# Kernel optimization log

Measured on AMD Instinct MI355X. Metric: run time of the kernel, lower is better.

Reference implementation:

```python
import jax, jax.numpy as jnp
import numpy as np
from jax import lax

B, D, K = 256, 128, 8192


def _conv_same(x, w, b):
    # x: [B,C,H,W], w: [O,I,3,3] (torch Conv2d layout), stride 1, padding 1 == SAME
    y = lax.conv_general_dilated(x, w, (1, 1), 'SAME',
                                 dimension_numbers=('NCHW', 'OIHW', 'NCHW'))
    return y + b[None, :, None, None]


def _convT_same(x, w, b):
    # torch ConvTranspose2d(k=3, stride=1, padding=1) with weight [I,O,3,3]
    # == SAME conv with spatially flipped kernel and swapped in/out channels
    wt = jnp.flip(w, axis=(2, 3)).transpose(1, 0, 2, 3)  # -> [O,I,3,3]
    return _conv_same(x, wt, b)


def setup_inputs() -> dict:
    key = jax.random.key(0)
    ks = jax.random.split(key, 12)
    s = 0.05
    return {
        'patch':  jax.random.normal(ks[0], (B, 3, 64, 64), jnp.float32),
        'enc_w1': jax.random.normal(ks[1], (64, 3, 3, 3), jnp.float32) * s,
        'enc_b1': jnp.zeros((64,), jnp.float32),
        'enc_w2': jax.random.normal(ks[2], (D, 64, 3, 3), jnp.float32) * s,
        'enc_b2': jnp.zeros((D,), jnp.float32),
        'emb':    jax.random.normal(ks[3], (K, D), jnp.float32),
        'dec_w1': jax.random.normal(ks[4], (D, 64, 3, 3), jnp.float32) * s,  # ConvT [in,out,k,k]
        'dec_b1': jnp.zeros((64,), jnp.float32),
        'dec_w2': jax.random.normal(ks[5], (64, 64, 3, 3), jnp.float32) * s,
        'dec_b2': jnp.zeros((64,), jnp.float32),
        'dec_w3': jax.random.normal(ks[6], (64, 3, 3, 3), jnp.float32) * s,
        'dec_b3': jnp.zeros((3,), jnp.float32),
    }


def reference(patch, enc_w1, enc_b1, enc_w2, enc_b2, emb,
              dec_w1, dec_b1, dec_w2, dec_b2, dec_w3, dec_b3):
    # ---- encode_patch ----
    h = jax.nn.relu(_conv_same(patch, enc_w1, enc_b1))
    h = _conv_same(h, enc_w2, enc_b2)
    z = jnp.mean(h, axis=(2, 3))  # AdaptiveAvgPool2d((1,1)) + flatten -> [B,D]

    # ---- VQ: cdist + argmin + gather ----
    # argmin over squared L2 == argmin over cdist(p=2); avoid sqrt.
    d2 = (jnp.sum(z * z, axis=1, keepdims=True)
          + jnp.sum(emb * emb, axis=1)[None, :]
          - 2.0 * z @ emb.T)  # [B,K]
    encoding_indices = jnp.argmin(d2, axis=1)  # [B]
    z_q = emb[encoding_indices]  # [B,D]

    commitment_loss = jnp.mean((lax.stop_gradient(z_q) - z) ** 2)
    codebook_loss = jnp.mean((z_q - lax.stop_gradient(z)) ** 2)

    # ---- decode_vector ----
    # bilinear interpolate of a 1x1 map to 64x64 is a pure broadcast
    v = jnp.broadcast_to(z_q[:, :, None, None], (z_q.shape[0], z_q.shape[1], 64, 64))
    d = jax.nn.relu(_convT_same(v, dec_w1, dec_b1))
    d = jax.nn.relu(_convT_same(d, dec_w2, dec_b2))
    recon = jnp.tanh(_convT_same(d, dec_w3, dec_b3))  # [B,3,64,64]

    return recon, codebook_loss, commitment_loss, encoding_indices[:, None]
```

## Files before the change

### kernel.cpp

```cpp
#include <hip/hip_runtime.h>
#include <math.h>

typedef float float4u __attribute__((ext_vector_type(4), aligned(4)));


__global__ __launch_bounds__(256) void k_conv1_pre(
    const float* __restrict__ patch, const float* __restrict__ w1,
    const float* __restrict__ b1, const float* __restrict__ dw1,
    const float* __restrict__ emb, float* __restrict__ pstat,
    float* __restrict__ Wcfg, float* __restrict__ en2)
{
    __shared__ __align__(16) float lds[2304];
    const int blk = blockIdx.x;
    const int tid = threadIdx.x;

    if (blk >= 2048) {
        const int gid = (blk - 2048) * 256 + tid;
        if (gid < 73728) {
            const int cfg = gid >> 13;
            const int o = (gid >> 7) & 63;
            const int i = gid & 127;
            const int cy = cfg / 3, cx = cfg % 3;
            const int ylo = (cy == 2) ? 1 : 0, yhi = (cy == 0) ? 1 : 2;
            const int xlo = (cx == 2) ? 1 : 0, xhi = (cx == 0) ? 1 : 2;
            const float* wp = dw1 + ((size_t)i * 64 + o) * 9;
            float s = 0.f;
            for (int ky = ylo; ky <= yhi; ++ky)
                for (int kx = xlo; kx <= xhi; ++kx)
                    s += wp[ky * 3 + kx];
            Wcfg[gid] = s;
        } else if (gid < 81920) {
            const int k = gid - 73728;
            const float4* e = (const float4*)(emb + (size_t)k * 128);
            float s = 0.f;
            for (int t = 0; t < 32; ++t) {
                float4 v = e[t];
                s = fmaf(v.x, v.x, fmaf(v.y, v.y, fmaf(v.z, v.z, fmaf(v.w, v.w, s))));
            }
            en2[k] = s;
        }
        return;
    }

    const int b = blk >> 3, rg = blk & 7;
    const int y0 = rg * 8;
    const float* pb = patch + (size_t)b * 12288;
    for (int i = tid; i < 2160; i += 256) {
        const int c = i / 720, rem = i - c * 720;
        const int r = rem / 72, p = rem - r * 72;
        const int y = y0 + r - 1, x = p - 3;
        float v = 0.f;
        if (y >= 0 && y < 64 && x >= 0 && x < 64)
            v = pb[(c << 12) + (y << 6) + x];
        lds[i] = v;
    }
    __syncthreads();

    const int ch = tid & 63, q = tid >> 6;
    float w[3][3][3];
#pragma unroll
    for (int ic = 0; ic < 3; ++ic)
#pragma unroll
        for (int ky = 0; ky < 3; ++ky)
#pragma unroll
            for (int kx = 0; kx < 3; ++kx)
                w[ic][ky][kx] = w1[((ch * 3 + ic) * 3 + ky) * 3 + kx];
    const float bias = b1[ch];

    float T = 0, r0s = 0, r63s = 0, c0s = 0, c63s = 0;
    float h00 = 0, h063 = 0, h630 = 0, h6363 = 0;

#pragma unroll
    for (int sub = 0; sub < 2; ++sub) {
        const int yl = q * 2 + sub;
        const bool isr0  = (rg == 0) && (yl == 0);
        const bool isr63 = (rg == 7) && (yl == 7);
        float cr[3][3][2];
#pragma unroll
        for (int ic = 0; ic < 3; ++ic)
#pragma unroll
            for (int ky = 0; ky < 3; ++ky) {
                const float2 t2 = *(const float2*)&lds[(ic * 10 + yl + ky) * 72 + 2];
                cr[ic][ky][0] = t2.x; cr[ic][ky][1] = t2.y;
            }
#pragma unroll 4
        for (int xc = 0; xc < 16; ++xc) {
            float a0 = bias, a1 = bias, a2 = bias, a3 = bias;
#pragma unroll
            for (int ic = 0; ic < 3; ++ic)
#pragma unroll
                for (int ky = 0; ky < 3; ++ky) {
                    const float4 nw = *(const float4*)&lds[(ic * 10 + yl + ky) * 72 + xc * 4 + 4];
                    const float w0 = w[ic][ky][0], w1v = w[ic][ky][1], w2v = w[ic][ky][2];
                    a0 = fmaf(w0, cr[ic][ky][0], fmaf(w1v, cr[ic][ky][1], fmaf(w2v, nw.x, a0)));
                    a1 = fmaf(w0, cr[ic][ky][1], fmaf(w1v, nw.x, fmaf(w2v, nw.y, a1)));
                    a2 = fmaf(w0, nw.x, fmaf(w1v, nw.y, fmaf(w2v, nw.z, a2)));
                    a3 = fmaf(w0, nw.y, fmaf(w1v, nw.z, fmaf(w2v, nw.w, a3)));
                    cr[ic][ky][0] = nw.z; cr[ic][ky][1] = nw.w;
                }
            a0 = fmaxf(a0, 0.f); a1 = fmaxf(a1, 0.f);
            a2 = fmaxf(a2, 0.f); a3 = fmaxf(a3, 0.f);
            const float rs = (a0 + a1) + (a2 + a3);
            T += rs;
            if (isr0)  { r0s += rs;  if (xc == 0) h00 = a0;  if (xc == 15) h063 = a3; }
            if (isr63) { r63s += rs; if (xc == 0) h630 = a0; if (xc == 15) h6363 = a3; }
            if (xc == 0)  c0s += a0;
            if (xc == 15) c63s += a3;
        }
    }
    __syncthreads();
    {
        const float st[9] = {T, r0s, r63s, c0s, c63s, h00, h063, h630, h6363};
#pragma unroll
        for (int s = 0; s < 9; ++s) lds[(s * 4 + q) * 64 + ch] = st[s];
    }
    __syncthreads();
    if (tid < 64) {
        float* pp = pstat + (size_t)blk * 576;
#pragma unroll
        for (int s = 0; s < 9; ++s)
            pp[s * 64 + tid] = (lds[(s * 4 + 0) * 64 + tid] + lds[(s * 4 + 1) * 64 + tid])
                             + (lds[(s * 4 + 2) * 64 + tid] + lds[(s * 4 + 3) * 64 + tid]);
    }
}

__global__ __launch_bounds__(256) void k_zred(
    const float* __restrict__ pstat, const float* __restrict__ w2,
    const float* __restrict__ b2, float* __restrict__ z, float* __restrict__ zn2)
{
    __shared__ float fst[576];
    __shared__ __align__(16) float Ssh[576];
    __shared__ float zp[256];
    __shared__ float red2[128];
    const int b = blockIdx.x, tid = threadIdx.x;

    const float* pp = pstat + (size_t)b * 8 * 576;
    for (int i = tid; i < 576; i += 256) {
        float s = 0.f;
#pragma unroll
        for (int g = 0; g < 8; ++g) s += pp[g * 576 + i];
        fst[i] = s;
    }
    __syncthreads();

    if (tid < 64) {
        const float Tt   = fst[0 * 64 + tid], R0  = fst[1 * 64 + tid], R63 = fst[2 * 64 + tid];
        const float C0   = fst[3 * 64 + tid], C63 = fst[4 * 64 + tid];
        const float H00  = fst[5 * 64 + tid], H063 = fst[6 * 64 + tid];
        const float H630 = fst[7 * 64 + tid], H6363 = fst[8 * 64 + tid];
#pragma unroll
        for (int ky = 0; ky < 3; ++ky) {
            const float rex = (ky == 0) ? R63 : (ky == 2 ? R0 : 0.f);
#pragma unroll
            for (int kx = 0; kx < 3; ++kx) {
                const float cex = (kx == 0) ? C63 : (kx == 2 ? C0 : 0.f);
                float corner = 0.f;
                if (ky == 0 && kx == 0) corner = H6363;
                if (ky == 0 && kx == 2) corner = H630;
                if (ky == 2 && kx == 0) corner = H063;
                if (ky == 2 && kx == 2) corner = H00;
                Ssh[tid * 9 + ky * 3 + kx] = (Tt - rex - cex + corner) * (1.f / 4096.f);
            }
        }
    }
    __syncthreads();

    const int oc = tid & 127, h = tid >> 7;
    const float4* Wv = (const float4*)(w2 + (size_t)oc * 576 + h * 288);
    const float4* Sv = (const float4*)(Ssh + h * 288);
    float acc = 0.f;
    for (int t = 0; t < 72; ++t) {
        const float4 w4 = Wv[t], s4 = Sv[t];
        acc = fmaf(w4.x, s4.x, acc);
        acc = fmaf(w4.y, s4.y, acc);
        acc = fmaf(w4.z, s4.z, acc);
        acc = fmaf(w4.w, s4.w, acc);
    }
    zp[tid] = acc;
    __syncthreads();
    if (tid < 128) {
        const float zv = b2[tid] + zp[tid] + zp[tid + 128];
        z[(size_t)b * 128 + tid] = zv;
        red2[tid] = zv * zv;
    }
    __syncthreads();
    if (tid < 64) {
        float v = red2[tid] + red2[tid + 64];
        v += __shfl_xor(v, 32); v += __shfl_xor(v, 16); v += __shfl_xor(v, 8);
        v += __shfl_xor(v, 4);  v += __shfl_xor(v, 2);  v += __shfl_xor(v, 1);
        if (tid == 0) zn2[b] = v;
    }
}

__global__ __launch_bounds__(256) void k_vq(
    const float* __restrict__ z, const float* __restrict__ emb,
    const float* __restrict__ en2, float* __restrict__ pd2, int* __restrict__ pidx)
{
    __shared__ __align__(16) float zsh[1024];
    __shared__ float wd[8][4];
    __shared__ int   wi[8][4];
    const int tid = threadIdx.x;
    const int bg = blockIdx.x >> 4, kc = blockIdx.x & 15;
    const int b0 = bg * 8;
    for (int i = tid; i < 1024; i += 256) zsh[i] = z[(size_t)b0 * 128 + i];
    __syncthreads();

    const int k0 = kc * 512 + tid, k1 = k0 + 256;
    const float4* e0 = (const float4*)(emb + (size_t)k0 * 128);
    const float4* e1 = (const float4*)(emb + (size_t)k1 * 128);
    const float4* zv = (const float4*)zsh;

    float acc0[8], acc1[8];
#pragma unroll
    for (int bb = 0; bb < 8; ++bb) { acc0[bb] = 0.f; acc1[bb] = 0.f; }

    for (int t = 0; t < 32; ++t) {
        const float4 ea = e0[t], eb = e1[t];
#pragma unroll
        for (int bb = 0; bb < 8; ++bb) {
            const float4 zz = zv[bb * 32 + t];
            acc0[bb] = fmaf(zz.x, ea.x, fmaf(zz.y, ea.y, fmaf(zz.z, ea.z, fmaf(zz.w, ea.w, acc0[bb]))));
            acc1[bb] = fmaf(zz.x, eb.x, fmaf(zz.y, eb.y, fmaf(zz.z, eb.z, fmaf(zz.w, eb.w, acc1[bb]))));
        }
    }
    const float E0 = en2[k0], E1 = en2[k1];
    const int wv_ = tid >> 6, ln = tid & 63;
#pragma unroll
    for (int bb = 0; bb < 8; ++bb) {
        const float da = fmaf(-2.f, acc0[bb], E0);
        const float db = fmaf(-2.f, acc1[bb], E1);
        float d; int ix;
        if (da <= db) { d = da; ix = k0; } else { d = db; ix = k1; }
#pragma unroll
        for (int off = 32; off > 0; off >>= 1) {
            const float od = __shfl_xor(d, off);
            const int   oi = __shfl_xor(ix, off);
            if (od < d || (od == d && oi < ix)) { d = od; ix = oi; }
        }
        if (ln == 0) { wd[bb][wv_] = d; wi[bb][wv_] = ix; }
    }
    __syncthreads();
    if (tid < 8) {
        float d = wd[tid][0]; int ix = wi[tid][0];
#pragma unroll
        for (int wv2 = 1; wv2 < 4; ++wv2) {
            const float od = wd[tid][wv2]; const int oi = wi[tid][wv2];
            if (od < d || (od == d && oi < ix)) { d = od; ix = oi; }
        }
        pd2[(b0 + tid) * 16 + kc] = d;
        pidx[(b0 + tid) * 16 + kc] = ix;
    }
}

__global__ __launch_bounds__(256) void k_decode(
    const float* __restrict__ emb, const float* __restrict__ zn2,
    const float* __restrict__ pd2, const int* __restrict__ pidx,
    const float* __restrict__ Wcfg, const float* __restrict__ db1,
    const float* __restrict__ dw2, const float* __restrict__ db2,
    const float* __restrict__ dw3, const float* __restrict__ db3,
    float* __restrict__ out)
{
    __shared__ __align__(16) float zsh[128];
    __shared__ float d1e[64][10];
    __shared__ float d2e[64][26];
    __shared__ float o3[3 * 49];
    __shared__ float dw3sh[1728];
    __shared__ float redl[256];
    __shared__ int bsel;

    const int b = blockIdx.x, tid = threadIdx.x;

    float dmin = pd2[tid * 16]; int bi = pidx[tid * 16];
    for (int j = 1; j < 16; ++j) {
        const float d = pd2[tid * 16 + j]; const int ix = pidx[tid * 16 + j];
        if (d < dmin || (d == dmin && ix < bi)) { dmin = d; bi = ix; }
    }
    if (tid == b) bsel = bi;
    redl[tid] = dmin + zn2[tid];
    __syncthreads();

    if (b == 0) out[3145730 + tid] = (float)bi;
    if (tid < 128) {
        redl[tid] += redl[tid + 128];
        zsh[tid] = emb[(size_t)bsel * 128 + tid];
    }
    for (int id = tid; id < 1728; id += 256) dw3sh[id] = dw3[id];
    if (tid < 64) { d1e[tid][9] = 0.f; d2e[tid][25] = 0.f; }
    __syncthreads();

    if (tid < 64) {
        float v = redl[tid] + redl[tid + 64];
        v += __shfl_xor(v, 32); v += __shfl_xor(v, 16); v += __shfl_xor(v, 8);
        v += __shfl_xor(v, 4);  v += __shfl_xor(v, 2);  v += __shfl_xor(v, 1);
        if (tid == 0 && b == 0) {
            const float L = v * (1.f / 32768.f);
            out[3145728] = L;
            out[3145729] = L;
        }
    }

    for (int id = tid; id < 576; id += 256) {
        const int o = id / 9, cfg = id - o * 9;
        const float4* wv = (const float4*)(Wcfg + ((size_t)cfg * 64 + o) * 128);
        const float4* zv = (const float4*)zsh;
        float acc = db1[o];
        for (int t = 0; t < 32; ++t) {
            const float4 w4 = wv[t], z4 = zv[t];
            acc = fmaf(w4.x, z4.x, acc);
            acc = fmaf(w4.y, z4.y, acc);
            acc = fmaf(w4.z, z4.z, acc);
            acc = fmaf(w4.w, z4.w, acc);
        }
        d1e[o][cfg] = fmaxf(acc, 0.f);
    }
    __syncthreads();

    {
        const int TY5[5][3] = {{-1,0,1},{0,1,1},{1,1,1},{1,1,2},{1,2,-1}};
        const int o = tid >> 2, isub = tid & 3;
        float acc[25];
#pragma unroll
        for (int cc = 0; cc < 25; ++cc) acc[cc] = 0.f;
        for (int ii = 0; ii < 16; ++ii) {
            const int i = isub + ii * 4;
            float d1v[10];
#pragma unroll
            for (int t = 0; t < 9; ++t) d1v[t] = d1e[i][t];
            d1v[9] = 0.f;
            const float* wp = dw2 + ((size_t)i * 64 + o) * 9;
            const float4u w03 = *(const float4u*)wp;
            const float4u w47 = *(const float4u*)(wp + 4);
            const float w8v = wp[8];
            const float w9[9] = {w03.x, w03.y, w03.z, w03.w, w47.x, w47.y, w47.z, w47.w, w8v};
#pragma unroll
            for (int cy = 0; cy < 5; ++cy) {
#pragma unroll
                for (int ky = 0; ky < 3; ++ky) {
                    const int ty = TY5[cy][ky];
                    if (ty < 0) continue;
#pragma unroll
                    for (int cx = 0; cx < 5; ++cx) {
#pragma unroll
                        for (int kx = 0; kx < 3; ++kx) {
                            const int tx = TY5[cx][kx];
                            if (tx < 0) continue;
                            acc[cy * 5 + cx] = fmaf(w9[(2 - ky) * 3 + (2 - kx)],
                                                    d1v[ty * 3 + tx], acc[cy * 5 + cx]);
                        }
                    }
                }
            }
        }
#pragma unroll
        for (int cc = 0; cc < 25; ++cc) {
            float v = acc[cc];
            v += __shfl_xor(v, 1);
            v += __shfl_xor(v, 2);
            if (isub == 0) d2e[o][cc] = fmaxf(v + db2[o], 0.f);
        }
    }
    __syncthreads();

    if (tid < 147) {
        const int TY7[7][3] = {{-1,0,1},{0,1,2},{1,2,2},{2,2,2},{2,2,3},{2,3,4},{3,4,-1}};
        const int c3 = tid / 49, cc = tid % 49, cy = cc / 7, cx = cc % 7;
        float acc = db3[c3];
        for (int i = 0; i < 64; ++i) {
            const float* wp = &dw3sh[(i * 3 + c3) * 9];
#pragma unroll
            for (int ky = 0; ky < 3; ++ky) {
                const int ty = TY7[cy][ky];
#pragma unroll
                for (int kx = 0; kx < 3; ++kx) {
                    const int tx = TY7[cx][kx];
                    const int t = (ty < 0 || tx < 0) ? 25 : ty * 5 + tx;
                    acc = fmaf(wp[(2 - ky) * 3 + (2 - kx)], d2e[i][t], acc);
                }
            }
        }
        o3[c3 * 49 + cc] = tanhf(acc);
    }
    __syncthreads();

    float4* ob = (float4*)(out + (size_t)b * 12288);
    for (int id = tid; id < 3072; id += 256) {
        const int base = id * 4;
        const int c = base >> 12, rem = base & 4095, y = rem >> 6, x0 = rem & 63;
        const int ry = (y <= 3) ? y : (y >= 60 ? y - 57 : 3);
        const float* row = &o3[c * 49 + ry * 7];
        float4 v;
        int x;
        x = x0 + 0; v.x = row[(x <= 3) ? x : (x >= 60 ? x - 57 : 3)];
        x = x0 + 1; v.y = row[(x <= 3) ? x : (x >= 60 ? x - 57 : 3)];
        x = x0 + 2; v.z = row[(x <= 3) ? x : (x >= 60 ? x - 57 : 3)];
        x = x0 + 3; v.w = row[(x <= 3) ? x : (x >= 60 ? x - 57 : 3)];
        ob[id] = v;
    }
}

extern "C" void kernel_launch(void* const* d_in, const int* in_sizes, int n_in,
                              void* d_out, int out_size, void* d_ws, size_t ws_size,
                              hipStream_t stream)
{
    const float* patch  = (const float*)d_in[0];
    const float* enc_w1 = (const float*)d_in[1];
    const float* enc_b1 = (const float*)d_in[2];
    const float* enc_w2 = (const float*)d_in[3];
    const float* enc_b2 = (const float*)d_in[4];
    const float* emb    = (const float*)d_in[5];
    const float* dec_w1 = (const float*)d_in[6];
    const float* dec_b1 = (const float*)d_in[7];
    const float* dec_w2 = (const float*)d_in[8];
    const float* dec_b2 = (const float*)d_in[9];
    const float* dec_w3 = (const float*)d_in[10];
    const float* dec_b3 = (const float*)d_in[11];

    float* out = (float*)d_out;
    float* ws  = (float*)d_ws;

    float* pstat = ws;
    float* z     = ws + 1179648;
    float* zn2   = ws + 1212416;
    float* pd2   = ws + 1212672;
    int*   pidx  = (int*)(ws + 1216768);
    float* Wcfg  = ws + 1220864;
    float* en2   = ws + 1294592;

    k_conv1_pre<<<dim3(2368), dim3(256), 0, stream>>>(patch, enc_w1, enc_b1, dec_w1,
                                                      emb, pstat, Wcfg, en2);
    k_zred<<<dim3(256), dim3(256), 0, stream>>>(pstat, enc_w2, enc_b2, z, zn2);
    k_vq<<<dim3(512), dim3(256), 0, stream>>>(z, emb, en2, pd2, pidx);
    k_decode<<<dim3(256), dim3(256), 0, stream>>>(emb, zn2, pd2, pidx, Wcfg, dec_b1,
                                                  dec_w2, dec_b2, dec_w3, dec_b3, out);
}
```

Measured before the change: 134.3 us.

## Fuse z reduction into VQ kernel and compute codebook norms inline

Merges the k_zred kernel into k_vq. Each VQ block now recomputes z for its 8 batch rows from the conv1 partial statistics and enc_w2, and block kc==0 writes zn2. The codebook squared norms are accumulated inside the distance loop, so the en2 precompute in the first kernel is dropped. This saves one launch and the z/en2 round trips through global memory. In exchange, the z reduction and projection is repeated 16 times per batch group, with much larger per-block LDS use and extra serial work ahead of the distance loop.

```diff
diff --git a/kernel.cpp b/kernel.cpp
--- a/kernel.cpp
+++ b/kernel.cpp
@@ -7,8 +7,7 @@
 __global__ __launch_bounds__(256) void k_conv1_pre(
     const float* __restrict__ patch, const float* __restrict__ w1,
     const float* __restrict__ b1, const float* __restrict__ dw1,
-    const float* __restrict__ emb, float* __restrict__ pstat,
-    float* __restrict__ Wcfg, float* __restrict__ en2)
+    float* __restrict__ pstat, float* __restrict__ Wcfg)
 {
     __shared__ __align__(16) float lds[2304];
     const int blk = blockIdx.x;
@@ -16,29 +15,18 @@
 
     if (blk >= 2048) {
         const int gid = (blk - 2048) * 256 + tid;
-        if (gid < 73728) {
-            const int cfg = gid >> 13;
-            const int o = (gid >> 7) & 63;
-            const int i = gid & 127;
-            const int cy = cfg / 3, cx = cfg % 3;
-            const int ylo = (cy == 2) ? 1 : 0, yhi = (cy == 0) ? 1 : 2;
-            const int xlo = (cx == 2) ? 1 : 0, xhi = (cx == 0) ? 1 : 2;
-            const float* wp = dw1 + ((size_t)i * 64 + o) * 9;
-            float s = 0.f;
-            for (int ky = ylo; ky <= yhi; ++ky)
-                for (int kx = xlo; kx <= xhi; ++kx)
-                    s += wp[ky * 3 + kx];
-            Wcfg[gid] = s;
-        } else if (gid < 81920) {
-            const int k = gid - 73728;
-            const float4* e = (const float4*)(emb + (size_t)k * 128);
-            float s = 0.f;
-            for (int t = 0; t < 32; ++t) {
-                float4 v = e[t];
-                s = fmaf(v.x, v.x, fmaf(v.y, v.y, fmaf(v.z, v.z, fmaf(v.w, v.w, s))));
-            }
-            en2[k] = s;
-        }
+        const int cfg = gid >> 13;
+        const int o = (gid >> 7) & 63;
+        const int i = gid & 127;
+        const int cy = cfg / 3, cx = cfg % 3;
+        const int ylo = (cy == 2) ? 1 : 0, yhi = (cy == 0) ? 1 : 2;
+        const int xlo = (cx == 2) ? 1 : 0, xhi = (cx == 0) ? 1 : 2;
+        const float* wp = dw1 + ((size_t)i * 64 + o) * 9;
+        float s = 0.f;
+        for (int ky = ylo; ky <= yhi; ++ky)
+            for (int kx = xlo; kx <= xhi; ++kx)
+                s += wp[ky * 3 + kx];
+        Wcfg[gid] = s;
         return;
     }
 
@@ -124,30 +112,40 @@
     }
 }
 
-__global__ __launch_bounds__(256) void k_zred(
+__global__ __launch_bounds__(256) void k_vq(
     const float* __restrict__ pstat, const float* __restrict__ w2,
-    const float* __restrict__ b2, float* __restrict__ z, float* __restrict__ zn2)
+    const float* __restrict__ b2, const float* __restrict__ emb,
+    float* __restrict__ zn2, float* __restrict__ pd2, int* __restrict__ pidx)
 {
-    __shared__ float fst[576];
-    __shared__ __align__(16) float Ssh[576];
-    __shared__ float zp[256];
-    __shared__ float red2[128];
-    const int b = blockIdx.x, tid = threadIdx.x;
-
-    const float* pp = pstat + (size_t)b * 8 * 576;
-    for (int i = tid; i < 576; i += 256) {
+    __shared__ float fst8[8][576];
+    __shared__ __align__(16) float Ssh8[8][576];
+    __shared__ __align__(16) float zsh[1024];
+    __shared__ float wd[8][4];
+    __shared__ int   wi[8][4];
+    const int tid = threadIdx.x;
+    const int bg = blockIdx.x >> 4, kc = blockIdx.x & 15;
+    const int b0 = bg * 8;
+
+    for (int i = tid; i < 4608; i += 256) {
+        const int bb = i / 576, j = i - bb * 576;
+        const float* pp = pstat + ((size_t)(b0 + bb) * 8) * 576 + j;
         float s = 0.f;
 #pragma unroll
-        for (int g = 0; g < 8; ++g) s += pp[g * 576 + i];
-        fst[i] = s;
-    }
-    __syncthreads();
-
-    if (tid < 64) {
-        const float Tt   = fst[0 * 64 + tid], R0  = fst[1 * 64 + tid], R63 = fst[2 * 64 + tid];
-        const float C0   = fst[3 * 64 + tid], C63 = fst[4 * 64 + tid];
-        const float H00  = fst[5 * 64 + tid], H063 = fst[6 * 64 + tid];
-        const float H630 = fst[7 * 64 + tid], H6363 = fst[8 * 64 + tid];
+        for (int g = 0; g < 8; ++g) s += pp[g * 576];
+        fst8[bb][j] = s;
+    }
+    __syncthreads();
+
+#pragma unroll
+    for (int pp2 = 0; pp2 < 2; ++pp2) {
+        const int t = tid + pp2 * 256;
+        const int bb = t >> 6, ch = t & 63;
+        const float* f = fst8[bb];
+        const float Tt   = f[0 * 64 + ch], R0  = f[1 * 64 + ch], R63 = f[2 * 64 + ch];
+        const float C0   = f[3 * 64 + ch], C63 = f[4 * 64 + ch];
+        const float H00  = f[5 * 64 + ch], H063 = f[6 * 64 + ch];
+        const float H630 = f[7 * 64 + ch], H6363 = f[8 * 64 + ch];
+        float* Sp = &Ssh8[bb][ch * 9];
 #pragma unroll
         for (int ky = 0; ky < 3; ++ky) {
             const float rex = (ky == 0) ? R63 : (ky == 2 ? R0 : 0.f);
@@ -159,51 +157,45 @@
                 if (ky == 0 && kx == 2) corner = H630;
                 if (ky == 2 && kx == 0) corner = H063;
                 if (ky == 2 && kx == 2) corner = H00;
-                Ssh[tid * 9 + ky * 3 + kx] = (Tt - rex - cex + corner) * (1.f / 4096.f);
+                Sp[ky * 3 + kx] = (Tt - rex - cex + corner) * (1.f / 4096.f);
             }
         }
     }
     __syncthreads();
 
-    const int oc = tid & 127, h = tid >> 7;
-    const float4* Wv = (const float4*)(w2 + (size_t)oc * 576 + h * 288);
-    const float4* Sv = (const float4*)(Ssh + h * 288);
-    float acc = 0.f;
-    for (int t = 0; t < 72; ++t) {
-        const float4 w4 = Wv[t], s4 = Sv[t];
-        acc = fmaf(w4.x, s4.x, acc);
-        acc = fmaf(w4.y, s4.y, acc);
-        acc = fmaf(w4.z, s4.z, acc);
-        acc = fmaf(w4.w, s4.w, acc);
-    }
-    zp[tid] = acc;
-    __syncthreads();
-    if (tid < 128) {
-        const float zv = b2[tid] + zp[tid] + zp[tid + 128];
-        z[(size_t)b * 128 + tid] = zv;
-        red2[tid] = zv * zv;
-    }
-    __syncthreads();
-    if (tid < 64) {
-        float v = red2[tid] + red2[tid + 64];
-        v += __shfl_xor(v, 32); v += __shfl_xor(v, 16); v += __shfl_xor(v, 8);
-        v += __shfl_xor(v, 4);  v += __shfl_xor(v, 2);  v += __shfl_xor(v, 1);
-        if (tid == 0) zn2[b] = v;
-    }
-}
-
-__global__ __launch_bounds__(256) void k_vq(
-    const float* __restrict__ z, const float* __restrict__ emb,
-    const float* __restrict__ en2, float* __restrict__ pd2, int* __restrict__ pidx)
-{
-    __shared__ __align__(16) float zsh[1024];
-    __shared__ float wd[8][4];
-    __shared__ int   wi[8][4];
-    const int tid = threadIdx.x;
-    const int bg = blockIdx.x >> 4, kc = blockIdx.x & 15;
-    const int b0 = bg * 8;
-    for (int i = tid; i < 1024; i += 256) zsh[i] = z[(size_t)b0 * 128 + i];
-    __syncthreads();
+    {
+        const int oc = tid & 127, half = tid >> 7;
+        const float4* Wv = (const float4*)(w2 + (size_t)oc * 576);
+        const float bv = b2[oc];
+#pragma unroll
+        for (int jb = 0; jb < 4; ++jb) {
+            const int bb = half * 4 + jb;
+            const float4* Sv = (const float4*)Ssh8[bb];
+            float acc = 0.f;
+            for (int t = 0; t < 144; ++t) {
+                const float4 w4 = Wv[t], s4 = Sv[t];
+                acc = fmaf(w4.x, s4.x, acc);
+                acc = fmaf(w4.y, s4.y, acc);
+                acc = fmaf(w4.z, s4.z, acc);
+                acc = fmaf(w4.w, s4.w, acc);
+            }
+            zsh[bb * 128 + oc] = bv + acc;
+        }
+    }
+    __syncthreads();
+
+    if (kc == 0) {
+        const int bb = tid >> 5, l = tid & 31;
+        float v = 0.f;
+#pragma unroll
+        for (int j = 0; j < 4; ++j) {
+            const float zv = zsh[bb * 128 + j * 32 + l];
+            v = fmaf(zv, zv, v);
+        }
+        v += __shfl_xor(v, 16); v += __shfl_xor(v, 8);
+        v += __shfl_xor(v, 4);  v += __shfl_xor(v, 2); v += __shfl_xor(v, 1);
+        if (l == 0) zn2[b0 + bb] = v;
+    }
 
     const int k0 = kc * 512 + tid, k1 = k0 + 256;
     const float4* e0 = (const float4*)(emb + (size_t)k0 * 128);
@@ -213,9 +205,12 @@
     float acc0[8], acc1[8];
 #pragma unroll
     for (int bb = 0; bb < 8; ++bb) { acc0[bb] = 0.f; acc1[bb] = 0.f; }
+    float s0 = 0.f, s1 = 0.f;
 
     for (int t = 0; t < 32; ++t) {
         const float4 ea = e0[t], eb = e1[t];
+        s0 = fmaf(ea.x, ea.x, fmaf(ea.y, ea.y, fmaf(ea.z, ea.z, fmaf(ea.w, ea.w, s0))));
+        s1 = fmaf(eb.x, eb.x, fmaf(eb.y, eb.y, fmaf(eb.z, eb.z, fmaf(eb.w, eb.w, s1))));
 #pragma unroll
         for (int bb = 0; bb < 8; ++bb) {
             const float4 zz = zv[bb * 32 + t];
@@ -223,12 +218,11 @@
             acc1[bb] = fmaf(zz.x, eb.x, fmaf(zz.y, eb.y, fmaf(zz.z, eb.z, fmaf(zz.w, eb.w, acc1[bb]))));
         }
     }
-    const float E0 = en2[k0], E1 = en2[k1];
     const int wv_ = tid >> 6, ln = tid & 63;
 #pragma unroll
     for (int bb = 0; bb < 8; ++bb) {
-        const float da = fmaf(-2.f, acc0[bb], E0);
-        const float db = fmaf(-2.f, acc1[bb], E1);
+        const float da = fmaf(-2.f, acc0[bb], s0);
+        const float db = fmaf(-2.f, acc1[bb], s1);
         float d; int ix;
         if (da <= db) { d = da; ix = k0; } else { d = db; ix = k1; }
 #pragma unroll
@@ -419,17 +413,15 @@
     float* ws  = (float*)d_ws;
 
     float* pstat = ws;
-    float* z     = ws + 1179648;
-    float* zn2   = ws + 1212416;
-    float* pd2   = ws + 1212672;
-    int*   pidx  = (int*)(ws + 1216768);
-    float* Wcfg  = ws + 1220864;
-    float* en2   = ws + 1294592;
-
-    k_conv1_pre<<<dim3(2368), dim3(256), 0, stream>>>(patch, enc_w1, enc_b1, dec_w1,
-                                                      emb, pstat, Wcfg, en2);
-    k_zred<<<dim3(256), dim3(256), 0, stream>>>(pstat, enc_w2, enc_b2, z, zn2);
-    k_vq<<<dim3(512), dim3(256), 0, stream>>>(z, emb, en2, pd2, pidx);
+    float* zn2   = ws + 1179648;
+    float* pd2   = ws + 1179904;
+    int*   pidx  = (int*)(ws + 1184000);
+    float* Wcfg  = ws + 1188096;
+
+    k_conv1_pre<<<dim3(2336), dim3(256), 0, stream>>>(patch, enc_w1, enc_b1, dec_w1,
+                                                      pstat, Wcfg);
+    k_vq<<<dim3(512), dim3(256), 0, stream>>>(pstat, enc_w2, enc_b2, emb,
+                                              zn2, pd2, pidx);
     k_decode<<<dim3(256), dim3(256), 0, stream>>>(emb, zn2, pd2, pidx, Wcfg, dec_b1,
                                                   dec_w2, dec_b2, dec_w3, dec_b3, out);
 }
```

Result: slower. 249.2 us (+85.6%).
